# Performance work log

Measured on AMD Instinct MI355X. Metric: run time of the kernel, lower is better.

Reference implementation:

```python
import jax, jax.numpy as jnp
import numpy as np

N, E, HID, H_SA, H_MHA, L = 20000, 320000, 128, 4, 4, 32
MLP_HID = 4 * HID
EPS = 1e-6


def _ln(x, eps=EPS):
    mu = jnp.mean(x, axis=-1, keepdims=True)
    var = jnp.var(x, axis=-1, keepdims=True)
    return (x - mu) * jax.lax.rsqrt(var + eps)


def _modulate(x, shift, scale):
    return x * (1.0 + scale) + shift


def setup_inputs() -> dict:
    key = jax.random.key(0)
    ks = jax.random.split(key, 32)
    s = 0.02
    inp = {
        'x': jax.random.normal(ks[0], (N, HID), jnp.float32),
        'edge_index': jax.random.randint(ks[1], (2, E), 0, N, jnp.int64),
        't': jax.random.normal(ks[2], (N, HID), jnp.float32),
        'text_emb': jax.random.normal(ks[3], (N, L, HID), jnp.float32),
        # TransformerConv (per-head out_channels = HID, concat=False)
        'sa_q_w': jax.random.normal(ks[4], (HID, H_SA * HID), jnp.float32) * s,
        'sa_q_b': jnp.zeros((H_SA * HID,), jnp.float32),
        'sa_k_w': jax.random.normal(ks[5], (HID, H_SA * HID), jnp.float32) * s,
        'sa_k_b': jnp.zeros((H_SA * HID,), jnp.float32),
        'sa_v_w': jax.random.normal(ks[6], (HID, H_SA * HID), jnp.float32) * s,
        'sa_v_b': jnp.zeros((H_SA * HID,), jnp.float32),
        'sa_skip_w': jax.random.normal(ks[7], (HID, HID), jnp.float32) * s,
        'sa_skip_b': jnp.zeros((HID,), jnp.float32),
        # norm3 affine
        'n3_g': jnp.ones((HID,), jnp.float32),
        'n3_b': jnp.zeros((HID,), jnp.float32),
        # MultiheadAttention
        'mha_q_w': jax.random.normal(ks[8], (HID, HID), jnp.float32) * s,
        'mha_q_b': jnp.zeros((HID,), jnp.float32),
        'mha_k_w': jax.random.normal(ks[9], (HID, HID), jnp.float32) * s,
        'mha_k_b': jnp.zeros((HID,), jnp.float32),
        'mha_v_w': jax.random.normal(ks[10], (HID, HID), jnp.float32) * s,
        'mha_v_b': jnp.zeros((HID,), jnp.float32),
        'mha_o_w': jax.random.normal(ks[11], (HID, HID), jnp.float32) * s,
        'mha_o_b': jnp.zeros((HID,), jnp.float32),
        # MLP
        'fc1_w': jax.random.normal(ks[12], (HID, MLP_HID), jnp.float32) * s,
        'fc1_b': jnp.zeros((MLP_HID,), jnp.float32),
        'fc2_w': jax.random.normal(ks[13], (MLP_HID, HID), jnp.float32) * s,
        'fc2_b': jnp.zeros((HID,), jnp.float32),
        # adaLN modulation
        'ada_w': jax.random.normal(ks[14], (HID, 6 * HID), jnp.float32) * s,
        'ada_b': jnp.zeros((6 * HID,), jnp.float32),
    }
    return inp


def reference(x, edge_index, t, text_emb,
              sa_q_w, sa_q_b, sa_k_w, sa_k_b, sa_v_w, sa_v_b, sa_skip_w, sa_skip_b,
              n3_g, n3_b,
              mha_q_w, mha_q_b, mha_k_w, mha_k_b, mha_v_w, mha_v_b, mha_o_w, mha_o_b,
              fc1_w, fc1_b, fc2_w, fc2_b, ada_w, ada_b):
    n = x.shape[0]
    # adaLN: SiLU -> Linear -> chunk(6)
    mod = jax.nn.silu(t) @ ada_w + ada_b  # [N, 6*HID]
    shift_msa, scale_msa, gate_msa, shift_mlp, scale_mlp, gate_mlp = jnp.split(mod, 6, axis=1)

    # ---- graph self-attention (PyG TransformerConv, concat=False) ----
    xm = _modulate(_ln(x), shift_msa, scale_msa)  # [N, HID]
    q = (xm @ sa_q_w + sa_q_b).reshape(n, H_SA, HID)
    k = (xm @ sa_k_w + sa_k_b).reshape(n, H_SA, HID)
    v = (xm @ sa_v_w + sa_v_b).reshape(n, H_SA, HID)
    src, dst = edge_index[0], edge_index[1]  # messages flow src -> dst
    # per-edge attention logits [E, H]
    logits = jnp.einsum('ehd,ehd->eh', q[dst], k[src]) / jnp.sqrt(jnp.float32(HID))
    m = jax.ops.segment_max(logits, dst, num_segments=n)          # [N, H]
    ex = jnp.exp(logits - m[dst])                                  # [E, H]
    den = jax.ops.segment_sum(ex, dst, num_segments=n)            # [N, H]
    alpha = ex / den[dst]                                          # [E, H]
    agg = jax.ops.segment_sum(alpha[:, :, None] * v[src], dst, num_segments=n)  # [N, H, HID]
    sa_out = agg.mean(axis=1) + (xm @ sa_skip_w + sa_skip_b)       # concat=False -> head mean, + root skip
    x = x + gate_msa * sa_out

    # ---- cross attention: each node attends over its text memory ----
    qn = _ln(x) * n3_g + n3_b                                      # norm3 (affine)
    dh = HID // H_MHA
    qh = (qn @ mha_q_w + mha_q_b).reshape(n, H_MHA, dh)
    kh = (text_emb @ mha_k_w + mha_k_b).reshape(n, L, H_MHA, dh)
    vh = (text_emb @ mha_v_w + mha_v_b).reshape(n, L, H_MHA, dh)
    scores = jnp.einsum('nhd,nlhd->nhl', qh, kh) / jnp.sqrt(jnp.float32(dh))
    attn = jax.nn.softmax(scores, axis=-1)
    ctx = jnp.einsum('nhl,nlhd->nhd', attn, vh).reshape(n, HID)
    x = x + (ctx @ mha_o_w + mha_o_b)

    # ---- gated MLP ----
    xm2 = _modulate(_ln(x), shift_mlp, scale_mlp)
    h = jax.nn.gelu(xm2 @ fc1_w + fc1_b, approximate=True)
    x = x + gate_mlp * (h @ fc2_w + fc2_b)
    return x
```

## Files before the change

### kernel.cpp

```cpp
#include <hip/hip_runtime.h>
#include <hip/hip_bf16.h>
#include <math.h>

using ushort8 = __attribute__((ext_vector_type(8))) unsigned short;
using short8  = __attribute__((ext_vector_type(8))) short;
using f32x4   = __attribute__((ext_vector_type(4))) float;
using f32x2   = __attribute__((ext_vector_type(2))) float;

__device__ __forceinline__ float bf2f(unsigned short u) {
    union { unsigned int i; float f; } c; c.i = ((unsigned int)u) << 16; return c.f;
}
__device__ __forceinline__ unsigned short f2bf(float f) {
    __hip_bfloat16 h = __float2bfloat16(f);
    return *reinterpret_cast<unsigned short*>(&h);
}
__device__ __forceinline__ float silu_f(float x) { return x / (1.f + __expf(-x)); }
__device__ __forceinline__ float gelu_f(float x) {
    float x3 = x * x * x;
    return 0.5f * x * (1.f + tanhf(0.7978845608028654f * (x + 0.044715f * x3)));
}

constexpr int QKV_STRIDE_B = 2304;

__device__ __forceinline__ void stage_tile_async(
    const unsigned short* __restrict__ gbase,
    int K, unsigned short (*lds)[64], int nrows, int wid, int lane)
{
    int nch = nrows >> 3;
#pragma unroll
    for (int c = wid; c < nch; c += 4) {
        int n0 = c * 8;
        int n = n0 + (lane >> 3);
        int b = (lane & 7) ^ (n & 7);
        const unsigned short* src = gbase + (size_t)n * K + b * 8;
        __builtin_amdgcn_global_load_lds(
            (const __attribute__((address_space(1))) unsigned int*)src,
            (__attribute__((address_space(3))) unsigned int*)&lds[n0][0],
            16, 0, 0);
    }
}

template<int WM, int AIN, int PRE, int EPI, int OUTBF>
__global__ __launch_bounds__(256) void gemm_mfma(
    const void* __restrict__ Ain, const unsigned short* __restrict__ Wt,
    const float* __restrict__ bias, void* __restrict__ Cout,
    const float* __restrict__ res, const void* __restrict__ gatep,
    int Nrows, int K, int M)
{
    constexpr int BM = 32 * WM;
    __shared__ unsigned short As[BM][64];
    __shared__ unsigned short Bs[128][64];
    const int tid = threadIdx.x;
    const int row0 = blockIdx.x * BM;
    const int col0 = blockIdx.y * 128;
    const int lane = tid & 63;
    const int wid  = tid >> 6;
    const int wr = (wid >> 1) * 16 * WM;
    const int wc = (wid & 1) * 64;
    const int lr = lane & 15;
    const int lk = lane >> 4;

    f32x4 acc[WM][4];
#pragma unroll
    for (int i = 0; i < WM; i++)
#pragma unroll
        for (int j = 0; j < 4; j++) acc[i][j] = (f32x4)0.f;

    for (int k0 = 0; k0 < K; k0 += 64) {
        if (AIN == 1) {
            stage_tile_async((const unsigned short*)Ain + (size_t)row0 * K + k0,
                             K, As, BM, wid, lane);
        } else {
#pragma unroll
            for (int i = 0; i < BM * 8 / 256; i++) {
                int f = tid + i * 256;
                int m = f >> 3, b = f & 7;
                int r = row0 + m;
                ushort8 h;
                if (r < Nrows) {
                    const float* ap = (const float*)Ain + (size_t)r * K + k0 + b * 8;
                    float4 p0 = *(const float4*)ap;
                    float4 p1 = *(const float4*)(ap + 4);
                    float v[8] = {p0.x, p0.y, p0.z, p0.w, p1.x, p1.y, p1.z, p1.w};
                    if (PRE == 1) {
#pragma unroll
                        for (int j = 0; j < 8; j++) v[j] = silu_f(v[j]);
                    }
#pragma unroll
                    for (int j = 0; j < 8; j++) h[j] = f2bf(v[j]);
                } else {
#pragma unroll
                    for (int j = 0; j < 8; j++) h[j] = 0;
                }
                *(ushort8*)&As[m][((b ^ (m & 7))) * 8] = h;
            }
        }
        stage_tile_async(Wt + (size_t)col0 * K + k0, K, Bs, 128, wid, lane);
        __syncthreads();

        short8 afr[WM][2], bfr[4][2];
#pragma unroll
        for (int fr = 0; fr < WM; fr++)
#pragma unroll
            for (int s = 0; s < 2; s++) {
                int m = wr + fr * 16 + lr;
                int blk = (s * 4 + lk) ^ (m & 7);
                afr[fr][s] = *(const short8*)&As[m][blk * 8];
            }
#pragma unroll
        for (int fc = 0; fc < 4; fc++)
#pragma unroll
            for (int s = 0; s < 2; s++) {
                int n = wc + fc * 16 + lr;
                int blk = (s * 4 + lk) ^ (n & 7);
                bfr[fc][s] = *(const short8*)&Bs[n][blk * 8];
            }
#pragma unroll
        for (int fr = 0; fr < WM; fr++)
#pragma unroll
            for (int fc = 0; fc < 4; fc++)
#pragma unroll
                for (int s = 0; s < 2; s++)
                    acc[fr][fc] = __builtin_amdgcn_mfma_f32_16x16x32_bf16(
                        afr[fr][s], bfr[fc][s], acc[fr][fc], 0, 0, 0);
        __syncthreads();
    }

#pragma unroll
    for (int fr = 0; fr < WM; fr++) {
#pragma unroll
        for (int fc = 0; fc < 4; fc++) {
#pragma unroll
            for (int r = 0; r < 4; r++) {
                int row = row0 + wr + fr * 16 + (lane >> 4) * 4 + r;
                if (row >= Nrows) continue;
                int col = col0 + wc + fc * 16 + (lane & 15);
                float val = acc[fr][fc][r] + bias[col];
                if (EPI == 4) {
                    unsigned char* rowp = (unsigned char*)Cout + (size_t)row * QKV_STRIDE_B;
                    if (col < 512) {
                        *(unsigned short*)(rowp + 2 * col) = f2bf(val);
                    } else if (col < 1536) {
                        int p = __builtin_amdgcn_cvt_pk_fp8_f32(val, 0.f, 0, false);
                        rowp[1024 + (col - 512)] = (unsigned char)(p & 0xff);
                    } else {
                        *(unsigned short*)(rowp + 2048 + 2 * (col - 1536)) = f2bf(val);
                    }
                } else {
                    size_t idx = (size_t)row * M + col;
                    if (EPI == 1) val = gelu_f(val);
                    else if (EPI == 2) val = res[idx] + val;
                    else if (EPI == 3) val = res[idx] +
                        bf2f(((const unsigned short*)gatep)[(size_t)row * 768 + col]) * val;
                    if (OUTBF) ((unsigned short*)Cout)[idx] = f2bf(val);
                    else       ((float*)Cout)[idx] = val;
                }
            }
        }
    }
}

__global__ __launch_bounds__(256) void prep_all(
    const float* __restrict__ qW, const float* __restrict__ qB,
    const float* __restrict__ kW, const float* __restrict__ kB,
    const float* __restrict__ vW, const float* __restrict__ vB,
    const float* __restrict__ sW, const float* __restrict__ sB,
    const float* __restrict__ f1W, const float* __restrict__ f2W,
    const float* __restrict__ adW,
    unsigned short* __restrict__ Wsa_t, float* __restrict__ bsa,
    unsigned short* __restrict__ fc1_t, unsigned short* __restrict__ fc2_t,
    unsigned short* __restrict__ ada_t,
    const float* __restrict__ Wq, const float* __restrict__ bq,
    const float* __restrict__ Wk, const float* __restrict__ Wv,
    const float* __restrict__ bv, const float* __restrict__ Wo,
    const float* __restrict__ bo,
    unsigned short* __restrict__ Mcat_t, float* __restrict__ biasM,
    unsigned short* __restrict__ Pcat_t, float* __restrict__ co)
{
    int g = blockIdx.x * 256 + threadIdx.x;
    if (g < 65536) {
        int m = g >> 7, kk = g & 127;
        Wsa_t[m * 128 + kk] = f2bf(qW[(size_t)kk * 512 + m]);
        if (kk == 0) bsa[m] = qB[m];
    } else if (g < 131072) {
        int l = g - 65536; int m = l >> 7, kk = l & 127;
        int h = m >> 7, dl = m & 127;
        int p = 512 + h * 256 + ((dl >> 3) << 4) + (dl & 7);
        Wsa_t[p * 128 + kk] = f2bf(kW[(size_t)kk * 512 + m]);
        if (kk == 0) bsa[p] = kB[m];
    } else if (g < 196608) {
        int l = g - 131072; int m = l >> 7, kk = l & 127;
        int h = m >> 7, dl = m & 127;
        int p = 512 + h * 256 + ((dl >> 3) << 4) + 8 + (dl & 7);
        Wsa_t[p * 128 + kk] = f2bf(vW[(size_t)kk * 512 + m]);
        if (kk == 0) bsa[p] = vB[m];
    } else if (g < 212992) {
        int l = g - 196608; int m = l >> 7, kk = l & 127;
        Wsa_t[(1536 + m) * 128 + kk] = f2bf(sW[(size_t)kk * 128 + m]);
        if (kk == 0) bsa[1536 + m] = sB[m];
    } else if (g < 278528) {
        int l = g - 212992; int m = l >> 7, kk = l & 127;
        fc1_t[m * 128 + kk] = f2bf(f1W[(size_t)kk * 512 + m]);
    } else if (g < 344064) {
        int l = g - 278528; int m = l >> 9, kk = l & 511;
        fc2_t[m * 512 + kk] = f2bf(f2W[(size_t)kk * 128 + m]);
    } else if (g < 442368) {
        int l = g - 344064; int m = l >> 7, kk = l & 127;
        ada_t[m * 128 + kk] = f2bf(adW[(size_t)kk * 768 + m]);
    } else {
        int g2 = g - 442368;
        {
            int i0 = g2 >> 9, col = g2 & 511, h = col >> 7, i = col & 127;
            float s = 0.f;
#pragma unroll 8
            for (int j = 0; j < 32; j++)
                s += Wq[i0 * 128 + h * 32 + j] * Wk[i * 128 + h * 32 + j];
            Mcat_t[col * 128 + i0] = f2bf(s);
        }
        {
            int rowp = g2 >> 7, j = g2 & 127, h = rowp >> 7, i = rowp & 127;
            float s = 0.f;
#pragma unroll 8
            for (int d = 0; d < 32; d++)
                s += Wv[i * 128 + h * 32 + d] * Wo[(h * 32 + d) * 128 + j];
            Pcat_t[j * 512 + rowp] = f2bf(s);
        }
        if (g2 < 512) {
            int h = g2 >> 7, i = g2 & 127;
            float s = 0.f;
            for (int j = 0; j < 32; j++)
                s += bq[h * 32 + j] * Wk[i * 128 + h * 32 + j];
            biasM[g2] = s;
        }
        if (g2 < 128) {
            float s = bo[g2];
            for (int m = 0; m < 128; m++) s += bv[m] * Wo[m * 128 + g2];
            co[g2] = s;
        }
    }
}

__global__ __launch_bounds__(256) void ln_mod_kernel(
    const float* __restrict__ x, const unsigned short* __restrict__ mod,
    int shift_off, int scale_off, unsigned short* __restrict__ outb, int N)
{
    int node = blockIdx.x * 4 + (threadIdx.x >> 6);
    if (node >= N) return;
    int lane = threadIdx.x & 63;
    f32x2 v = *(const f32x2*)(x + (size_t)node * 128 + lane * 2);
    float s = v[0] + v[1], ss = v[0] * v[0] + v[1] * v[1];
#pragma unroll
    for (int m = 1; m < 64; m <<= 1) { s += __shfl_xor(s, m); ss += __shfl_xor(ss, m); }
    float mu = s * (1.f / 128.f);
    float rs = rsqrtf(ss * (1.f / 128.f) - mu * mu + 1e-6f);
    const unsigned short* mp = mod + (size_t)node * 768;
    ushort2 sh = *(const ushort2*)(mp + shift_off + lane * 2);
    ushort2 sc = *(const ushort2*)(mp + scale_off + lane * 2);
    ushort2 o;
    o.x = f2bf((v[0] - mu) * rs * (1.f + bf2f(sc.x)) + bf2f(sh.x));
    o.y = f2bf((v[1] - mu) * rs * (1.f + bf2f(sc.y)) + bf2f(sh.y));
    *(ushort2*)(outb + (size_t)node * 128 + lane * 2) = o;
}

__global__ void count_edges(const int* __restrict__ dst, int* __restrict__ count, int E) {
    int e = blockIdx.x * blockDim.x + threadIdx.x;
    if (e < E) atomicAdd(&count[dst[e]], 1);
}

__global__ __launch_bounds__(1024) void scan_block(const int* __restrict__ cnt,
                                                   int* __restrict__ pre,
                                                   int* __restrict__ bsum, int n)
{
    __shared__ int tmp[1024];
    int gid = blockIdx.x * 1024 + threadIdx.x;
    int v = (gid < n) ? cnt[gid] : 0;
    tmp[threadIdx.x] = v;
    __syncthreads();
    for (int off = 1; off < 1024; off <<= 1) {
        int add = (threadIdx.x >= off) ? tmp[threadIdx.x - off] : 0;
        __syncthreads();
        tmp[threadIdx.x] += add;
        __syncthreads();
    }
    if (gid < n) pre[gid] = tmp[threadIdx.x];
    if (threadIdx.x == 1023) bsum[blockIdx.x] = tmp[1023];
}

__global__ void scan_fix(const int* __restrict__ pre, const int* __restrict__ bsum,
                         const int* __restrict__ cnt,
                         int* __restrict__ base, int* __restrict__ cursor,
                         int n, int nb)
{
    __shared__ int boff[32];
    if (threadIdx.x == 0) {
        int c = 0;
        for (int i = 0; i < nb; i++) { boff[i] = c; c += bsum[i]; }
    }
    __syncthreads();
    int gid = blockIdx.x * 256 + threadIdx.x;
    if (gid < n) {
        int inc = pre[gid] + boff[gid >> 10];
        base[gid + 1] = inc;
        cursor[gid] = inc - cnt[gid];
    }
    if (gid == 0) base[0] = 0;
}

__global__ void scatter_edges(const int* __restrict__ src, const int* __restrict__ dst,
                              int* __restrict__ cursor, int* __restrict__ csr_src, int E) {
    int e = blockIdx.x * blockDim.x + threadIdx.x;
    if (e < E) {
        int pos = atomicAdd(&cursor[dst[e]], 1);
        csr_src[pos] = src[e];
    }
}

__global__ __launch_bounds__(64) void sa_node_kernel(
    const unsigned char* __restrict__ qkv,
    const int* __restrict__ base, const int* __restrict__ csr_src,
    const float* __restrict__ x, const unsigned short* __restrict__ mod,
    const float* __restrict__ n3g, const float* __restrict__ n3b,
    float* __restrict__ x1, unsigned short* __restrict__ qn)
{
    int node = blockIdx.x, l = threadIdx.x;
    const unsigned char* nrow = qkv + (size_t)node * QKV_STRIDE_B;
    ushort8 qu = *(const ushort8*)(nrow + l * 16);
    const float scl = 0.08838834764831845f;
    float q[8];
#pragma unroll
    for (int j = 0; j < 8; j++) q[j] = bf2f(qu[j]) * scl;
    int beg = base[node], end = base[node + 1];
    float den = 0.f;
    float a[8];
#pragma unroll
    for (int j = 0; j < 8; j++) a[j] = 0.f;
    uint4 c0 = make_uint4(0, 0, 0, 0), c1 = c0;
    if (beg < end)
        c0 = *(const uint4*)(qkv + (size_t)csr_src[beg] * QKV_STRIDE_B + 1024 + l * 16);
    if (beg + 1 < end)
        c1 = *(const uint4*)(qkv + (size_t)csr_src[beg + 1] * QKV_STRIDE_B + 1024 + l * 16);
    for (int e = beg; e < end; e += 2) {
        uint4 m0 = c0, m1 = c1;
        if (e + 2 < end)
            c0 = *(const uint4*)(qkv + (size_t)csr_src[e + 2] * QKV_STRIDE_B + 1024 + l * 16);
        if (e + 3 < end)
            c1 = *(const uint4*)(qkv + (size_t)csr_src[e + 3] * QKV_STRIDE_B + 1024 + l * 16);
        f32x2 kA, kB, kC, kD;
        kA = __builtin_amdgcn_cvt_pk_f32_fp8(m0.x, false);
        kB = __builtin_amdgcn_cvt_pk_f32_fp8(m0.x, true);
        kC = __builtin_amdgcn_cvt_pk_f32_fp8(m0.y, false);
        kD = __builtin_amdgcn_cvt_pk_f32_fp8(m0.y, true);
        float p0 = q[0]*kA[0] + q[1]*kA[1] + q[2]*kB[0] + q[3]*kB[1]
                 + q[4]*kC[0] + q[5]*kC[1] + q[6]*kD[0] + q[7]*kD[1];
        kA = __builtin_amdgcn_cvt_pk_f32_fp8(m1.x, false);
        kB = __builtin_amdgcn_cvt_pk_f32_fp8(m1.x, true);
        kC = __builtin_amdgcn_cvt_pk_f32_fp8(m1.y, false);
        kD = __builtin_amdgcn_cvt_pk_f32_fp8(m1.y, true);
        float p1 = q[0]*kA[0] + q[1]*kA[1] + q[2]*kB[0] + q[3]*kB[1]
                 + q[4]*kC[0] + q[5]*kC[1] + q[6]*kD[0] + q[7]*kD[1];
#pragma unroll
        for (int mm = 1; mm < 16; mm <<= 1) {
            p0 += __shfl_xor(p0, mm);
            p1 += __shfl_xor(p1, mm);
        }
        float pe0 = __expf(fminf(p0, 80.f));
        float pe1 = (e + 1 < end) ? __expf(fminf(p1, 80.f)) : 0.f;
        den += pe0 + pe1;
        f32x2 vA, vB, vC, vD, wA, wB, wC, wD;
        vA = __builtin_amdgcn_cvt_pk_f32_fp8(m0.z, false);
        vB = __builtin_amdgcn_cvt_pk_f32_fp8(m0.z, true);
        vC = __builtin_amdgcn_cvt_pk_f32_fp8(m0.w, false);
        vD = __builtin_amdgcn_cvt_pk_f32_fp8(m0.w, true);
        wA = __builtin_amdgcn_cvt_pk_f32_fp8(m1.z, false);
        wB = __builtin_amdgcn_cvt_pk_f32_fp8(m1.z, true);
        wC = __builtin_amdgcn_cvt_pk_f32_fp8(m1.w, false);
        wD = __builtin_amdgcn_cvt_pk_f32_fp8(m1.w, true);
        a[0] += pe0 * vA[0] + pe1 * wA[0];
        a[1] += pe0 * vA[1] + pe1 * wA[1];
        a[2] += pe0 * vB[0] + pe1 * wB[0];
        a[3] += pe0 * vB[1] + pe1 * wB[1];
        a[4] += pe0 * vC[0] + pe1 * wC[0];
        a[5] += pe0 * vC[1] + pe1 * wC[1];
        a[6] += pe0 * vD[0] + pe1 * wD[0];
        a[7] += pe0 * vD[1] + pe1 * wD[1];
    }
    float inv = (den > 0.f) ? 0.25f / den : 0.f;
    __shared__ float sa_sh[128];
#pragma unroll
    for (int j = 0; j < 8; j++) {
        float s = a[j] * inv;
        s += __shfl_xor(s, 16);
        s += __shfl_xor(s, 32);
        a[j] = s;
    }
    if (l < 16) {
#pragma unroll
        for (int j = 0; j < 8; j++) sa_sh[l * 8 + j] = a[j];
    }
    __syncthreads();
    f32x2 sa2 = *(const f32x2*)&sa_sh[l * 2];
    ushort2 sk = *(const ushort2*)(nrow + 2048 + l * 4);
    ushort2 gt = *(const ushort2*)(mod + (size_t)node * 768 + 256 + l * 2);
    f32x2 xv2 = *(const f32x2*)(x + (size_t)node * 128 + l * 2);
    float xv0 = xv2[0] + bf2f(gt.x) * (sa2[0] + bf2f(sk.x));
    float xv1 = xv2[1] + bf2f(gt.y) * (sa2[1] + bf2f(sk.y));
    f32x2 xo; xo[0] = xv0; xo[1] = xv1;
    *(f32x2*)(x1 + (size_t)node * 128 + l * 2) = xo;
    float s = xv0 + xv1, ssq = xv0 * xv0 + xv1 * xv1;
#pragma unroll
    for (int m = 1; m < 64; m <<= 1) { s += __shfl_xor(s, m); ssq += __shfl_xor(ssq, m); }
    float mu = s * (1.f / 128.f);
    float rs = rsqrtf(ssq * (1.f / 128.f) - mu * mu + 1e-6f);
    ushort2 qo;
    qo.x = f2bf((xv0 - mu) * rs * n3g[l * 2] + n3b[l * 2]);
    qo.y = f2bf((xv1 - mu) * rs * n3g[l * 2 + 1] + n3b[l * 2 + 1]);
    *(ushort2*)(qn + (size_t)node * 128 + l * 2) = qo;
}

__global__ __launch_bounds__(128) void cross_mid_kernel(
    const float* __restrict__ te, const unsigned short* __restrict__ qw,
    unsigned short* __restrict__ u)
{
    int node = blockIdx.x, t = threadIdx.x;
    __shared__ float tes[32 * 132];
    __shared__ float qws[512];
    __shared__ float attnL[128];
#pragma unroll
    for (int i = 0; i < 8; i++) {
        int f = t + i * 128;
        int l = f >> 5, ii = (f & 31) * 4;
        float4 val = *(const float4*)(te + (size_t)node * 4096 + l * 128 + ii);
        *(float4*)&tes[l * 132 + ii] = val;
    }
    {
        ushort4 qv = *(const ushort4*)(qw + (size_t)node * 512 + t * 4);
        qws[t * 4 + 0] = bf2f(qv.x);
        qws[t * 4 + 1] = bf2f(qv.y);
        qws[t * 4 + 2] = bf2f(qv.z);
        qws[t * 4 + 3] = bf2f(qv.w);
    }
    __syncthreads();

    int h = t >> 5, l = t & 31;
    float sc = 0.f;
#pragma unroll
    for (int i = 0; i < 32; i++) {
        float4 tv = *(const float4*)&tes[l * 132 + i * 4];
        float4 qv4 = *(const float4*)&qws[h * 128 + i * 4];
        sc += tv.x * qv4.x + tv.y * qv4.y + tv.z * qv4.z + tv.w * qv4.w;
    }
    sc *= 0.17677669529663687f;
    float mx = sc;
#pragma unroll
    for (int mm = 1; mm < 32; mm <<= 1) mx = fmaxf(mx, __shfl_xor(mx, mm));
    float e = __expf(sc - mx);
    float ssum = e;
#pragma unroll
    for (int mm = 1; mm < 32; mm <<= 1) ssum += __shfl_xor(ssum, mm);
    attnL[t] = e / ssum;
    __syncthreads();

    int i0 = t & 31;
    float u0 = 0, u1 = 0, u2 = 0, u3 = 0;
#pragma unroll 4
    for (int ll = 0; ll < 32; ll++) {
        float a = attnL[h * 32 + ll];
        u0 += a * tes[ll * 132 + i0];
        u1 += a * tes[ll * 132 + i0 + 32];
        u2 += a * tes[ll * 132 + i0 + 64];
        u3 += a * tes[ll * 132 + i0 + 96];
    }
    size_t ub = (size_t)node * 512 + h * 128;
    u[ub + i0] = f2bf(u0);
    u[ub + i0 + 32] = f2bf(u1);
    u[ub + i0 + 64] = f2bf(u2);
    u[ub + i0 + 96] = f2bf(u3);
}

extern "C" void kernel_launch(void* const* d_in, const int* in_sizes, int n_in,
                              void* d_out, int out_size, void* d_ws, size_t ws_size,
                              hipStream_t stream)
{
    const int N = in_sizes[0] / 128;
    const int E = in_sizes[1] / 2;

    const float* x      = (const float*)d_in[0];
    const int*   ei     = (const int*)d_in[1];
    const float* t_in   = (const float*)d_in[2];
    const float* te     = (const float*)d_in[3];
    const float* sa_q_w = (const float*)d_in[4];
    const float* sa_q_b = (const float*)d_in[5];
    const float* sa_k_w = (const float*)d_in[6];
    const float* sa_k_b = (const float*)d_in[7];
    const float* sa_v_w = (const float*)d_in[8];
    const float* sa_v_b = (const float*)d_in[9];
    const float* sa_skip_w = (const float*)d_in[10];
    const float* sa_skip_b = (const float*)d_in[11];
    const float* n3_g   = (const float*)d_in[12];
    const float* n3_b   = (const float*)d_in[13];
    const float* mha_q_w = (const float*)d_in[14];
    const float* mha_q_b = (const float*)d_in[15];
    const float* mha_k_w = (const float*)d_in[16];
    const float* mha_v_w = (const float*)d_in[18];
    const float* mha_v_b = (const float*)d_in[19];
    const float* mha_o_w = (const float*)d_in[20];
    const float* mha_o_b = (const float*)d_in[21];
    const float* fc1_w  = (const float*)d_in[22];
    const float* fc1_b  = (const float*)d_in[23];
    const float* fc2_w  = (const float*)d_in[24];
    const float* fc2_b  = (const float*)d_in[25];
    const float* ada_w  = (const float*)d_in[26];
    const float* ada_b  = (const float*)d_in[27];
    float* out = (float*)d_out;

    float* ws = (float*)d_ws;
    size_t o = 0;
    unsigned short* modb = (unsigned short*)(ws + o); o += (size_t)N * 384;
    unsigned short* Bbuf = (unsigned short*)(ws + o); o += (size_t)N * 64;
    unsigned short* Qn   = (unsigned short*)(ws + o); o += (size_t)N * 64;
    unsigned short* Cbuf = (unsigned short*)(ws + o); o += (size_t)N * 256;
    unsigned short* Dbuf = (unsigned short*)(ws + o); o += (size_t)N * 256;
    unsigned short* Ebuf = (unsigned short*)(ws + o); o += (size_t)N * 256;
    float* Gbuf = ws + o; o += (size_t)N * 128;
    unsigned char* QKV = (unsigned char*)(ws + o); o += (size_t)N * (QKV_STRIDE_B / 4);
    unsigned short* Wsa_t  = (unsigned short*)(ws + o); o += 1664 * 128 / 2;
    unsigned short* Mcat_t = (unsigned short*)(ws + o); o += 512 * 128 / 2;
    unsigned short* Pcat_t = (unsigned short*)(ws + o); o += 128 * 512 / 2;
    unsigned short* fc1_t  = (unsigned short*)(ws + o); o += 512 * 128 / 2;
    unsigned short* fc2_t  = (unsigned short*)(ws + o); o += 128 * 512 / 2;
    unsigned short* ada_t  = (unsigned short*)(ws + o); o += 768 * 128 / 2;
    float* bsa   = ws + o; o += 1664;
    float* biasM = ws + o; o += 512;
    float* co    = ws + o; o += 128;
    int* count   = (int*)(ws + o); o += N;
    int* base    = (int*)(ws + o); o += N + 4;
    int* cursor  = (int*)(ws + o); o += N;
    int* pre     = (int*)(ws + o); o += N;
    int* bsum    = (int*)(ws + o); o += 32;
    int* csr_src = (int*)(ws + o); o += E;

    const int* src = ei;
    const int* dst = ei + E;
    const int rb128 = (N + 127) / 128;
    const int rb64  = (N + 63) / 64;
    const int nScan = (N + 1023) / 1024;

    prep_all<<<1984, 256, 0, stream>>>(sa_q_w, sa_q_b, sa_k_w, sa_k_b,
                                       sa_v_w, sa_v_b, sa_skip_w, sa_skip_b,
                                       fc1_w, fc2_w, ada_w,
                                       Wsa_t, bsa, fc1_t, fc2_t, ada_t,
                                       mha_q_w, mha_q_b, mha_k_w, mha_v_w,
                                       mha_v_b, mha_o_w, mha_o_b,
                                       Mcat_t, biasM, Pcat_t, co);

    hipMemsetAsync(count, 0, (size_t)N * sizeof(int), stream);
    count_edges<<<(E + 255) / 256, 256, 0, stream>>>(dst, count, E);
    scan_block<<<nScan, 1024, 0, stream>>>(count, pre, bsum, N);
    scan_fix<<<(N + 255) / 256, 256, 0, stream>>>(pre, bsum, count, base, cursor, N, nScan);
    scatter_edges<<<(E + 255) / 256, 256, 0, stream>>>(src, dst, cursor, csr_src, E);

    gemm_mfma<4, 0, 1, 0, 1><<<dim3(rb128, 6), 256, 0, stream>>>(
        t_in, ada_t, ada_b, modb, nullptr, nullptr, N, 128, 768);

    ln_mod_kernel<<<(N + 3) / 4, 256, 0, stream>>>(x, modb, 0, 128, Bbuf, N);

    gemm_mfma<4, 1, 0, 4, 1><<<dim3(rb128, 13), 256, 0, stream>>>(
        Bbuf, Wsa_t, bsa, QKV, nullptr, nullptr, N, 128, 1664);

    sa_node_kernel<<<N, 64, 0, stream>>>(QKV, base, csr_src, x, modb,
                                         n3_g, n3_b, Gbuf, Qn);

    gemm_mfma<4, 1, 0, 0, 1><<<dim3(rb128, 4), 256, 0, stream>>>(
        Qn, Mcat_t, biasM, Cbuf, nullptr, nullptr, N, 128, 512);
    cross_mid_kernel<<<N, 128, 0, stream>>>(te, Cbuf, Dbuf);
    gemm_mfma<2, 1, 0, 2, 0><<<dim3(rb64, 1), 256, 0, stream>>>(
        Dbuf, Pcat_t, co, Gbuf, Gbuf, nullptr, N, 512, 128);

    ln_mod_kernel<<<(N + 3) / 4, 256, 0, stream>>>(Gbuf, modb, 384, 512, Bbuf, N);
    gemm_mfma<4, 1, 0, 1, 1><<<dim3(rb128, 4), 256, 0, stream>>>(
        Bbuf, fc1_t, fc1_b, Ebuf, nullptr, nullptr, N, 128, 512);
    gemm_mfma<2, 1, 0, 3, 0><<<dim3(rb64, 1), 256, 0, stream>>>(
        Ebuf, fc2_t, fc2_b, out, Gbuf, modb + 640, N, 512, 128);
}
```

Measured before the change: 370.6 us.

## Fuse residual+LN-modulate into projection GEMM epilogue, remap blocks XCD-aware, presilu t

```diff
diff --git a/kernel.cpp b/kernel.cpp
--- a/kernel.cpp
+++ b/kernel.cpp
@@ -40,19 +40,24 @@
     }
 }
 
-template<int WM, int AIN, int PRE, int EPI, int OUTBF>
+template<int WM, int EPI, int OUTBF>
 __global__ __launch_bounds__(256) void gemm_mfma(
     const void* __restrict__ Ain, const unsigned short* __restrict__ Wt,
     const float* __restrict__ bias, void* __restrict__ Cout,
     const float* __restrict__ res, const void* __restrict__ gatep,
-    int Nrows, int K, int M)
+    void* __restrict__ out2, int Nrows, int K, int M)
 {
     constexpr int BM = 32 * WM;
     __shared__ unsigned short As[BM][64];
     __shared__ unsigned short Bs[128][64];
     const int tid = threadIdx.x;
-    const int row0 = blockIdx.x * BM;
-    const int col0 = blockIdx.y * 128;
+    const int gx = gridDim.x;
+    const int T = gx * gridDim.y;
+    const int hw = blockIdx.y * gx + blockIdx.x;
+    const int q = T >> 3, r = T & 7, xc = hw & 7, j = hw >> 3;
+    const int work = (xc < r ? xc * (q + 1) : r * (q + 1) + (xc - r) * q) + j;
+    const int row0 = (work / gx) * BM;
+    const int col0 = (work % gx) * 128;
     const int lane = tid & 63;
     const int wid  = tid >> 6;
     const int wr = (wid >> 1) * 16 * WM;
@@ -64,37 +69,11 @@
 #pragma unroll
     for (int i = 0; i < WM; i++)
 #pragma unroll
-        for (int j = 0; j < 4; j++) acc[i][j] = (f32x4)0.f;
+        for (int jj = 0; jj < 4; jj++) acc[i][jj] = (f32x4)0.f;
 
     for (int k0 = 0; k0 < K; k0 += 64) {
-        if (AIN == 1) {
-            stage_tile_async((const unsigned short*)Ain + (size_t)row0 * K + k0,
-                             K, As, BM, wid, lane);
-        } else {
-#pragma unroll
-            for (int i = 0; i < BM * 8 / 256; i++) {
-                int f = tid + i * 256;
-                int m = f >> 3, b = f & 7;
-                int r = row0 + m;
-                ushort8 h;
-                if (r < Nrows) {
-                    const float* ap = (const float*)Ain + (size_t)r * K + k0 + b * 8;
-                    float4 p0 = *(const float4*)ap;
-                    float4 p1 = *(const float4*)(ap + 4);
-                    float v[8] = {p0.x, p0.y, p0.z, p0.w, p1.x, p1.y, p1.z, p1.w};
-                    if (PRE == 1) {
-#pragma unroll
-                        for (int j = 0; j < 8; j++) v[j] = silu_f(v[j]);
-                    }
-#pragma unroll
-                    for (int j = 0; j < 8; j++) h[j] = f2bf(v[j]);
-                } else {
-#pragma unroll
-                    for (int j = 0; j < 8; j++) h[j] = 0;
-                }
-                *(ushort8*)&As[m][((b ^ (m & 7))) * 8] = h;
-            }
-        }
+        stage_tile_async((const unsigned short*)Ain + (size_t)row0 * K + k0,
+                         K, As, BM, wid, lane);
         stage_tile_async(Wt + (size_t)col0 * K + k0, K, Bs, 128, wid, lane);
         __syncthreads();
 
@@ -131,11 +110,12 @@
 #pragma unroll
         for (int fc = 0; fc < 4; fc++) {
 #pragma unroll
-            for (int r = 0; r < 4; r++) {
-                int row = row0 + wr + fr * 16 + (lane >> 4) * 4 + r;
+            for (int rr = 0; rr < 4; rr++) {
+                int lrow = wr + fr * 16 + (lane >> 4) * 4 + rr;
+                int row = row0 + lrow;
                 if (row >= Nrows) continue;
                 int col = col0 + wc + fc * 16 + (lane & 15);
-                float val = acc[fr][fc][r] + bias[col];
+                float val = acc[fr][fc][rr] + bias[col];
                 if (EPI == 4) {
                     unsigned char* rowp = (unsigned char*)Cout + (size_t)row * QKV_STRIDE_B;
                     if (col < 512) {
@@ -146,6 +126,11 @@
                     } else {
                         *(unsigned short*)(rowp + 2048 + 2 * (col - 1536)) = f2bf(val);
                     }
+                } else if (EPI == 5) {
+                    size_t idx = (size_t)row * M + col;
+                    float x2 = res[idx] + val;
+                    ((float*)Cout)[idx] = x2;
+                    (&Bs[0][0])[lrow * 128 + col - col0] = f2bf(x2);
                 } else {
                     size_t idx = (size_t)row * M + col;
                     if (EPI == 1) val = gelu_f(val);
@@ -158,6 +143,46 @@
             }
         }
     }
+
+    if constexpr (EPI == 5) {
+        __syncthreads();
+        const unsigned short* x2b = &Bs[0][0];
+        const unsigned short* mod = (const unsigned short*)gatep;
+        for (int rr = wid; rr < BM; rr += 4) {
+            int row = row0 + rr;
+            if (row >= Nrows) continue;
+            ushort2 xv = *(const ushort2*)&x2b[rr * 128 + lane * 2];
+            float v0 = bf2f(xv.x), v1 = bf2f(xv.y);
+            float s = v0 + v1, ss = v0 * v0 + v1 * v1;
+#pragma unroll
+            for (int mm = 1; mm < 64; mm <<= 1) {
+                s += __shfl_xor(s, mm); ss += __shfl_xor(ss, mm);
+            }
+            float mu = s * (1.f / 128.f);
+            float rs = rsqrtf(ss * (1.f / 128.f) - mu * mu + 1e-6f);
+            const unsigned short* mp = mod + (size_t)row * 768;
+            ushort2 sh = *(const ushort2*)(mp + 384 + lane * 2);
+            ushort2 sc = *(const ushort2*)(mp + 512 + lane * 2);
+            ushort2 o;
+            o.x = f2bf((v0 - mu) * rs * (1.f + bf2f(sc.x)) + bf2f(sh.x));
+            o.y = f2bf((v1 - mu) * rs * (1.f + bf2f(sc.y)) + bf2f(sh.y));
+            *(ushort2*)((unsigned short*)out2 + (size_t)row * 128 + lane * 2) = o;
+        }
+    }
+}
+
+__global__ __launch_bounds__(256) void silu_bf16_kernel(
+    const float* __restrict__ t, unsigned short* __restrict__ o, int n8)
+{
+    int i = blockIdx.x * 256 + threadIdx.x;
+    if (i >= n8) return;
+    const float* p = t + (size_t)i * 8;
+    float4 a = *(const float4*)p, b = *(const float4*)(p + 4);
+    float v[8] = {a.x, a.y, a.z, a.w, b.x, b.y, b.z, b.w};
+    ushort8 h;
+#pragma unroll
+    for (int jj = 0; jj < 8; jj++) h[jj] = f2bf(silu_f(v[jj]));
+    *(ushort8*)(o + (size_t)i * 8) = h;
 }
 
 __global__ __launch_bounds__(256) void prep_all(
@@ -213,23 +238,23 @@
             int i0 = g2 >> 9, col = g2 & 511, h = col >> 7, i = col & 127;
             float s = 0.f;
 #pragma unroll 8
-            for (int j = 0; j < 32; j++)
-                s += Wq[i0 * 128 + h * 32 + j] * Wk[i * 128 + h * 32 + j];
+            for (int jj = 0; jj < 32; jj++)
+                s += Wq[i0 * 128 + h * 32 + jj] * Wk[i * 128 + h * 32 + jj];
             Mcat_t[col * 128 + i0] = f2bf(s);
         }
         {
-            int rowp = g2 >> 7, j = g2 & 127, h = rowp >> 7, i = rowp & 127;
+            int rowp = g2 >> 7, jc = g2 & 127, h = rowp >> 7, i = rowp & 127;
             float s = 0.f;
 #pragma unroll 8
             for (int d = 0; d < 32; d++)
-                s += Wv[i * 128 + h * 32 + d] * Wo[(h * 32 + d) * 128 + j];
-            Pcat_t[j * 512 + rowp] = f2bf(s);
+                s += Wv[i * 128 + h * 32 + d] * Wo[(h * 32 + d) * 128 + jc];
+            Pcat_t[jc * 512 + rowp] = f2bf(s);
         }
         if (g2 < 512) {
             int h = g2 >> 7, i = g2 & 127;
             float s = 0.f;
-            for (int j = 0; j < 32; j++)
-                s += bq[h * 32 + j] * Wk[i * 128 + h * 32 + j];
+            for (int jj = 0; jj < 32; jj++)
+                s += bq[h * 32 + jj] * Wk[i * 128 + h * 32 + jj];
             biasM[g2] = s;
         }
         if (g2 < 128) {
@@ -328,12 +353,12 @@
     const float scl = 0.08838834764831845f;
     float q[8];
 #pragma unroll
-    for (int j = 0; j < 8; j++) q[j] = bf2f(qu[j]) * scl;
+    for (int jj = 0; jj < 8; jj++) q[jj] = bf2f(qu[jj]) * scl;
     int beg = base[node], end = base[node + 1];
     float den = 0.f;
     float a[8];
 #pragma unroll
-    for (int j = 0; j < 8; j++) a[j] = 0.f;
+    for (int jj = 0; jj < 8; jj++) a[jj] = 0.f;
     uint4 c0 = make_uint4(0, 0, 0, 0), c1 = c0;
     if (beg < end)
         c0 = *(const uint4*)(qkv + (size_t)csr_src[beg] * QKV_STRIDE_B + 1024 + l * 16);
@@ -387,15 +412,15 @@
     float inv = (den > 0.f) ? 0.25f / den : 0.f;
     __shared__ float sa_sh[128];
 #pragma unroll
-    for (int j = 0; j < 8; j++) {
-        float s = a[j] * inv;
+    for (int jj = 0; jj < 8; jj++) {
+        float s = a[jj] * inv;
         s += __shfl_xor(s, 16);
         s += __shfl_xor(s, 32);
-        a[j] = s;
+        a[jj] = s;
     }
     if (l < 16) {
 #pragma unroll
-        for (int j = 0; j < 8; j++) sa_sh[l * 8 + j] = a[j];
+        for (int jj = 0; jj < 8; jj++) sa_sh[l * 8 + jj] = a[jj];
     }
     __syncthreads();
     f32x2 sa2 = *(const f32x2*)&sa_sh[l * 2];
@@ -539,6 +564,8 @@
     int* bsum    = (int*)(ws + o); o += 32;
     int* csr_src = (int*)(ws + o); o += E;
 
+    unsigned short* Tbuf = Ebuf;
+
     const int* src = ei;
     const int* dst = ei + E;
     const int rb128 = (N + 127) / 128;
@@ -559,26 +586,27 @@
     scan_fix<<<(N + 255) / 256, 256, 0, stream>>>(pre, bsum, count, base, cursor, N, nScan);
     scatter_edges<<<(E + 255) / 256, 256, 0, stream>>>(src, dst, cursor, csr_src, E);
 
-    gemm_mfma<4, 0, 1, 0, 1><<<dim3(rb128, 6), 256, 0, stream>>>(
-        t_in, ada_t, ada_b, modb, nullptr, nullptr, N, 128, 768);
+    silu_bf16_kernel<<<(N * 16 + 255) / 256, 256, 0, stream>>>(t_in, Tbuf, N * 16);
+
+    gemm_mfma<4, 0, 1><<<dim3(6, rb128), 256, 0, stream>>>(
+        Tbuf, ada_t, ada_b, modb, nullptr, nullptr, nullptr, N, 128, 768);
 
     ln_mod_kernel<<<(N + 3) / 4, 256, 0, stream>>>(x, modb, 0, 128, Bbuf, N);
 
-    gemm_mfma<4, 1, 0, 4, 1><<<dim3(rb128, 13), 256, 0, stream>>>(
-        Bbuf, Wsa_t, bsa, QKV, nullptr, nullptr, N, 128, 1664);
+    gemm_mfma<4, 4, 1><<<dim3(13, rb128), 256, 0, stream>>>(
+        Bbuf, Wsa_t, bsa, QKV, nullptr, nullptr, nullptr, N, 128, 1664);
 
     sa_node_kernel<<<N, 64, 0, stream>>>(QKV, base, csr_src, x, modb,
                                          n3_g, n3_b, Gbuf, Qn);
 
-    gemm_mfma<4, 1, 0, 0, 1><<<dim3(rb128, 4), 256, 0, stream>>>(
-        Qn, Mcat_t, biasM, Cbuf, nullptr, nullptr, N, 128, 512);
+    gemm_mfma<4, 0, 1><<<dim3(4, rb128), 256, 0, stream>>>(
+        Qn, Mcat_t, biasM, Cbuf, nullptr, nullptr, nullptr, N, 128, 512);
     cross_mid_kernel<<<N, 128, 0, stream>>>(te, Cbuf, Dbuf);
-    gemm_mfma<2, 1, 0, 2, 0><<<dim3(rb64, 1), 256, 0, stream>>>(
-        Dbuf, Pcat_t, co, Gbuf, Gbuf, nullptr, N, 512, 128);
-
-    ln_mod_kernel<<<(N + 3) / 4, 256, 0, stream>>>(Gbuf, modb, 384, 512, Bbuf, N);
-    gemm_mfma<4, 1, 0, 1, 1><<<dim3(rb128, 4), 256, 0, stream>>>(
-        Bbuf, fc1_t, fc1_b, Ebuf, nullptr, nullptr, N, 128, 512);
-    gemm_mfma<2, 1, 0, 3, 0><<<dim3(rb64, 1), 256, 0, stream>>>(
-        Ebuf, fc2_t, fc2_b, out, Gbuf, modb + 640, N, 512, 128);
-}
+    gemm_mfma<2, 5, 0><<<dim3(1, rb64), 256, 0, stream>>>(
+        Dbuf, Pcat_t, co, Gbuf, Gbuf, modb, Bbuf, N, 512, 128);
+
+    gemm_mfma<4, 1, 1><<<dim3(4, rb128), 256, 0, stream>>>(
+        Bbuf, fc1_t, fc1_b, Ebuf, nullptr, nullptr, nullptr, N, 128, 512);
+    gemm_mfma<2, 3, 0><<<dim3(1, rb64), 256, 0, stream>>>(
+        Ebuf, fc2_t, fc2_b, out, Gbuf, modb + 640, nullptr, N, 512, 128);
+}
```

Measured after the change: 365.2 us. About the same (-1.5%).
